# Performance work log

Measured on AMD Instinct MI355X. Metric: run time of the kernel, lower is better.

The kernel has to match this reference:

```python
import jax, jax.numpy as jnp
import numpy as np

N_HEAD = 16
T0 = 1.0        # eta schedule reference time
C_LOG = 3.0     # fixed eta(t) = C_LOG * log(t / T0)  (mode='log', non-learnable default)
ETA_CLIP = 50.0 # eta clamped to [-ETA_CLIP, ETA_CLIP] before exponentiation


def setup_inputs() -> dict:
    key = jax.random.key(0)
    k0, k1, k2 = jax.random.split(key, 3)
    B, T, D = 2, 2048, 1024
    x = jax.random.normal(k0, (B, T, D), dtype=jnp.float32)
    ln_weight = jnp.ones((D,), dtype=jnp.float32)  # LayerNorm weight (bias=False per cfg)
    c_attn_w = jax.random.normal(k1, (3 * D, D), dtype=jnp.float32) * 0.02  # torch Linear weight [3D, D]
    c_proj_w = jax.random.normal(k2, (D, D), dtype=jnp.float32) * 0.02      # output proj [D, D]
    # theta_h = inv_softplus(1.0) so that step size h = softplus(theta_h) = 1.0
    theta_h = jnp.asarray(np.log(np.expm1(1.0)), dtype=jnp.float32)
    return {"x": x, "ln_weight": ln_weight, "c_attn_w": c_attn_w,
            "c_proj_w": c_proj_w, "theta_h": theta_h}


def _layer_norm(x, w, eps=1e-5):
    mu = jnp.mean(x, axis=-1, keepdims=True)
    var = jnp.var(x, axis=-1, keepdims=True)
    return (x - mu) * jax.lax.rsqrt(var + eps) * w


def reference(x, ln_weight, c_attn_w, c_proj_w, theta_h):
    B, T, D = x.shape
    H = N_HEAD
    hd = D // H

    y = _layer_norm(x, ln_weight)
    qkv = jnp.einsum('btd,ed->bte', y, c_attn_w)        # [B, T, 3D]
    q, k, v = jnp.split(qkv, 3, axis=-1)
    q = q.reshape(B, T, H, hd).transpose(0, 2, 1, 3)    # [B, H, T, hd]
    k = k.reshape(B, T, H, hd).transpose(0, 2, 1, 3)
    v = v.reshape(B, T, H, hd).transpose(0, 2, 1, 3)

    # time-dependent conformal/symplectic scaling: t_i = t0 + h*i, eta = c_log*log(t/t0)
    h = jax.nn.softplus(theta_h)
    t = T0 + h * jnp.arange(T, dtype=jnp.float32)
    eta = jnp.clip(C_LOG * jnp.log(t / T0), -ETA_CLIP, ETA_CLIP)  # [T]
    q = q * jnp.exp(eta)[None, None, :, None]    # query scaled by exp(+eta(t_i))
    k = k * jnp.exp(-eta)[None, None, :, None]   # key scaled by exp(-eta(t_j))

    att = jnp.einsum('bhqd,bhkd->bhqk', q, k) / jnp.sqrt(jnp.float32(hd))
    mask = jnp.tril(jnp.ones((T, T), dtype=bool))  # causal: keep j <= i
    att = jnp.where(mask[None, None], att, -jnp.inf)
    att = jax.nn.softmax(att, axis=-1)

    out = jnp.einsum('bhqk,bhkd->bhqd', att, v)
    out = out.transpose(0, 2, 1, 3).reshape(B, T, D)
    return jnp.einsum('btd,ed->bte', out, c_proj_w)
```

## Files before the change

kernel.cpp:

```cpp
#include <hip/hip_runtime.h>
#include <stdint.h>
#include <stddef.h>

typedef __attribute__((ext_vector_type(8))) short short8;
typedef __attribute__((ext_vector_type(4))) float float4v;

#define T_SEQ 2048
#define D_MODEL 1024
#define NH 16
#define HD 64

static __device__ __forceinline__ unsigned short f2bf(float f) {
  unsigned u = __builtin_bit_cast(unsigned, f);
  u += 0x7fffu + ((u >> 16) & 1u);
  return (unsigned short)(u >> 16);
}
static __device__ __forceinline__ float bf2f(unsigned short h) {
  unsigned u = ((unsigned)h) << 16;
  return __builtin_bit_cast(float, u);
}
static __device__ __forceinline__ float4v mfma16(short8 a, short8 b, float4v c) {
  return __builtin_amdgcn_mfma_f32_16x16x32_bf16(a, b, c, 0, 0, 0);
}
static __device__ __forceinline__ void split3(float f, unsigned short& h0,
                                              unsigned short& h1, unsigned short& h2) {
  h0 = f2bf(f);
  float r1 = f - bf2f(h0);
  h1 = f2bf(r1);
  float r2 = r1 - bf2f(h1);
  h2 = f2bf(r2);
}
static __device__ __forceinline__ void split2(float f, unsigned short& h0, unsigned short& h1) {
  h0 = f2bf(f);
  h1 = f2bf(f - bf2f(h0));
}

static __device__ __forceinline__ void stage16(const unsigned short* g, unsigned short* l) {
#if __has_builtin(__builtin_amdgcn_global_load_lds)
  __builtin_amdgcn_global_load_lds(
      (const __attribute__((address_space(1))) unsigned int*)g,
      (__attribute__((address_space(3))) unsigned int*)l, 16, 0, 0);
#else
  *(short8*)l = *(const short8*)g;
#endif
}

__global__ __launch_bounds__(256) void prep_kernel(
    const float* x, const float* wgt, const float* attn_w, const float* theta,
    unsigned short* y0, unsigned short* y1, unsigned short* y2,
    unsigned short* W0, unsigned short* W1, unsigned short* W2,
    float* E, float* Einv) {
  __shared__ float rs[4], rq[4];
  int bx = blockIdx.x;
  int tid = threadIdx.x;
  if (bx < 4096) {
    int row = bx;
    const float* xr = x + (size_t)row * D_MODEL;
    float v[4];
    float sum = 0.f, ssq = 0.f;
    for (int it = 0; it < 4; ++it) {
      float f = xr[tid + 256 * it];
      v[it] = f;
      sum += f; ssq += f * f;
    }
    for (int off = 32; off >= 1; off >>= 1) {
      sum += __shfl_xor(sum, off, 64);
      ssq += __shfl_xor(ssq, off, 64);
    }
    int w = tid >> 6;
    if ((tid & 63) == 0) { rs[w] = sum; rq[w] = ssq; }
    __syncthreads();
    sum = rs[0] + rs[1] + rs[2] + rs[3];
    ssq = rq[0] + rq[1] + rq[2] + rq[3];
    float mu = sum * (1.0f / D_MODEL);
    float var = ssq * (1.0f / D_MODEL) - mu * mu;
    float rstd = rsqrtf(var + 1e-5f);
    for (int it = 0; it < 4; ++it) {
      int d = tid + 256 * it;
      float y = (v[it] - mu) * rstd * wgt[d];
      unsigned short h0, h1, h2;
      split3(y, h0, h1, h2);
      size_t o = (size_t)row * D_MODEL + d;
      y0[o] = h0; y1[o] = h1; y2[o] = h2;
    }
  } else if (bx < 5632) {
    size_t base = ((size_t)(bx - 4096) * 256 + tid) * 8;
    int row = (int)(base >> 10);
    short8 a, b, c;
    for (int j = 0; j < 8; ++j) {
      unsigned short h0, h1, h2;
      split3(attn_w[base + j], h0, h1, h2);
      a[j] = (short)h0; b[j] = (short)h1; c[j] = (short)h2;
    }
    *(short8*)(W0 + base) = a;
    *(short8*)(W1 + base) = b;
    if (row < 2048) *(short8*)(W2 + base) = c;
  } else {
    int i = (bx - 5632) * 256 + tid;
    if (i < T_SEQ) {
      float th = theta[0];
      float h = log1pf(expf(th));
      float t = 1.0f + h * (float)i;
      float eta = 3.0f * logf(t);
      eta = fminf(fmaxf(eta, -50.0f), 50.0f);
      E[i] = expf(eta);
      Einv[i] = expf(-eta);
    }
  }
}

__global__ __launch_bounds__(256) void conv_pw(const float* src, unsigned short* P0,
                                               unsigned short* P1) {
  size_t base = ((size_t)blockIdx.x * 256 + threadIdx.x) * 8;
  short8 a, b;
  for (int j = 0; j < 8; ++j) {
    unsigned short h0, h1;
    split2(src[base + j], h0, h1);
    a[j] = (short)h0; b[j] = (short)h1;
  }
  *(short8*)(P0 + base) = a;
  *(short8*)(P1 + base) = b;
}


#define RD_A(BUF, MF)                                                           \
  (*(const short8*)(lds_u + (BUF) * 12288 + (wm * 64 + (MF) * 16 + ln) * 32 +   \
                    slot8))
#define RD_B(BUF, NF)                                                           \
  (*(const short8*)(lds_u + (BUF) * 12288 + 8192 +                              \
                    (wn * 64 + (NF) * 16 + ln) * 32 + slot8))

#define STG(BUF, AP, BP, KI)                                                    \
  do {                                                                          \
    const unsigned short* ga = (AP) + (size_t)(m0 + srow) * 1024 + (KI) + kswz8; \
    stage16(ga, lds_u + (BUF) * 12288 + tid * 8);                               \
    stage16(ga + 128 * 1024, lds_u + (BUF) * 12288 + 4096 + tid * 8);           \
    stage16((BP) + (size_t)(brow0 + srow) * 1024 + (KI) + kswz8,                \
            lds_u + (BUF) * 12288 + 8192 + tid * 8);                            \
  } while (0)

#define ASEL(tb) ((tb) == 5 ? y2 : (((tb) & 1) ? y1 : y0))
#define BSEL(tb) (isV ? ((tb) < 2 ? W0 : W1)                                    \
                      : ((tb) < 2 ? W0 : ((tb) < 4 ? W1 : ((tb) == 4 ? W2 : W0))))

#define SBAR __builtin_amdgcn_s_barrier()
#define SCHED0 __builtin_amdgcn_sched_barrier(0)

#define PHASE(BUF, PBUF)                                                        \
  {                                                                             \
    short8 a0 = RD_A(BUF, 0), a1 = RD_A(BUF, 1);                                \
    short8 a2 = RD_A(BUF, 2), a3 = RD_A(BUF, 3);                                \
    short8 b0 = RD_B(BUF, 0), b1 = RD_B(BUF, 1);                                \
    short8 b2 = RD_B(BUF, 2), b3 = RD_B(BUF, 3);                                \
    bool pref = (t + 2 < NKT);                                                  \
    if (pref) {                                                                 \
      int tt = t + 2, tb = tt >> 5, ki = (tt & 31) << 5;                        \
      const unsigned short* Ap = ASEL(tb);                                      \
      const unsigned short* Bp = BSEL(tb);                                      \
      STG(PBUF, Ap, Bp, ki);                                                    \
    }                                                                           \
    SCHED0; SBAR;                                                               \
    asm volatile("s_waitcnt lgkmcnt(0)" ::: "memory");                          \
    SCHED0;                                                                     \
    __builtin_amdgcn_s_setprio(1);                                              \
    acc[0][0] = mfma16(a0, b0, acc[0][0]);                                      \
    acc[0][1] = mfma16(a0, b1, acc[0][1]);                                      \
    acc[0][2] = mfma16(a0, b2, acc[0][2]);                                      \
    acc[0][3] = mfma16(a0, b3, acc[0][3]);                                      \
    acc[1][0] = mfma16(a1, b0, acc[1][0]);                                      \
    acc[1][1] = mfma16(a1, b1, acc[1][1]);                                      \
    acc[1][2] = mfma16(a1, b2, acc[1][2]);                                      \
    acc[1][3] = mfma16(a1, b3, acc[1][3]);                                      \
    acc[2][0] = mfma16(a2, b0, acc[2][0]);                                      \
    acc[2][1] = mfma16(a2, b1, acc[2][1]);                                      \
    acc[2][2] = mfma16(a2, b2, acc[2][2]);                                      \
    acc[2][3] = mfma16(a2, b3, acc[2][3]);                                      \
    acc[3][0] = mfma16(a3, b0, acc[3][0]);                                      \
    acc[3][1] = mfma16(a3, b1, acc[3][1]);                                      \
    acc[3][2] = mfma16(a3, b2, acc[3][2]);                                      \
    acc[3][3] = mfma16(a3, b3, acc[3][3]);                                      \
    __builtin_amdgcn_s_setprio(0);                                              \
    SCHED0;                                                                     \
    if (pref) { asm volatile("s_waitcnt vmcnt(3)" ::: "memory"); }              \
    else      { asm volatile("s_waitcnt vmcnt(0)" ::: "memory"); }              \
    SBAR;                                                                       \
    ++t;                                                                        \
  }

__global__ __launch_bounds__(512, 4) void qkv_ring(
    const unsigned short* __restrict__ y0, const unsigned short* __restrict__ y1,
    const unsigned short* __restrict__ y2, const unsigned short* __restrict__ W0,
    const unsigned short* __restrict__ W1, const unsigned short* __restrict__ W2,
    const float* __restrict__ E, const float* __restrict__ Einv,
    float* __restrict__ Qf, unsigned short* __restrict__ K0,
    unsigned short* __restrict__ K1, unsigned short* __restrict__ K2,
    unsigned short* __restrict__ VbT) {
  extern __shared__ unsigned short lds_u[];
  int tid = threadIdx.x;
  int w = tid >> 6, lane = tid & 63, q4 = lane >> 4, ln = lane & 15;
  int wm = w >> 1, wn = w & 1;
  int slot8 = (q4 ^ ((ln >> 1) & 3)) * 8;
  int srow = tid >> 2;
  int kswz8 = ((tid & 3) ^ ((srow >> 1) & 3)) * 8;

  int bid = blockIdx.x, bx, by;
  if (bid < 256) {
    int wg = ((bid & 7) << 5) | (bid >> 3);
    by = wg >> 4; bx = wg & 15;
  } else {
    int vid = bid - 256;
    int wg = ((vid & 7) << 4) | (vid >> 3);
    by = wg >> 3; bx = 16 + (wg & 7);
  }
  int m0 = by * 256;
  bool isV = (bx >= 16);
  int NKT = isV ? 96 : 192;
  int brow0 = isV ? (2048 + (bx - 16) * 128) : bx * 128;

  float4v zero = {0.f, 0.f, 0.f, 0.f};
  float4v acc[4][4];
#pragma unroll
  for (int mf = 0; mf < 4; ++mf)
#pragma unroll
    for (int nf = 0; nf < 4; ++nf) acc[mf][nf] = zero;

  {
    const unsigned short* Ap = ASEL(0);
    const unsigned short* Bp = BSEL(0);
    STG(0, Ap, Bp, 0);
    STG(1, Ap, Bp, 32);
  }
  asm volatile("s_waitcnt vmcnt(3)" ::: "memory");
  SBAR;

  int t = 0;
  int nit = NKT / 3;
  for (int it = 0; it < nit; ++it) {
    PHASE(0, 2)
    PHASE(1, 0)
    PHASE(2, 1)
  }

  int bi = m0 >> 11, m0g = m0 & 2047;
  if (bx < 8) {
    float* Ql = (float*)lds_u;
    for (int g = 0; g < 2; ++g) {
      if (wn == g) {
#pragma unroll
        for (int mf = 0; mf < 4; ++mf)
#pragma unroll
          for (int nf = 0; nf < 4; ++nf)
#pragma unroll
            for (int r = 0; r < 4; ++r) {
              int rl = wm * 64 + mf * 16 + q4 * 4 + r;
              int tg = m0g + rl;
              Ql[rl * 64 + nf * 16 + ln] = acc[mf][nf][r] * (E[tg] * 0.1803368801f);
            }
      }
      __syncthreads();
      int h = bx * 2 + g;
      float* dst = Qf + ((size_t)(bi * NH + h) * T_SEQ + m0g) * HD;
      for (int itc = 0; itc < 8; ++itc) {
        int idx = itc * 512 + tid;
        *(float4v*)(dst + idx * 4) = *(const float4v*)(Ql + idx * 4);
      }
      __syncthreads();
    }
  } else if (bx < 16) {
    unsigned short* Kl = lds_u;
    for (int g = 0; g < 2; ++g)
      for (int half = 0; half < 2; ++half) {
        if (wn == g && (wm >> 1) == half) {
#pragma unroll
          for (int mf = 0; mf < 4; ++mf)
#pragma unroll
            for (int nf = 0; nf < 4; ++nf)
#pragma unroll
              for (int r = 0; r < 4; ++r) {
                int rlh = (wm & 1) * 64 + mf * 16 + q4 * 4 + r;
                int tg = m0g + half * 128 + rlh;
                unsigned short h0, h1, h2;
                split3(acc[mf][nf][r] * Einv[tg], h0, h1, h2);
                int o = rlh * 64 + nf * 16 + ln;
                Kl[o] = h0; Kl[8192 + o] = h1; Kl[16384 + o] = h2;
              }
        }
        __syncthreads();
        int h = (bx - 8) * 2 + g;
        size_t base = ((size_t)(bi * NH + h) * T_SEQ + m0g + half * 128) * HD;
        for (int itc = 0; itc < 2; ++itc) {
          int idx = itc * 512 + tid;
          *(short8*)(K0 + base + idx * 8) = *(const short8*)(Kl + idx * 8);
          *(short8*)(K1 + base + idx * 8) = *(const short8*)(Kl + 8192 + idx * 8);
          *(short8*)(K2 + base + idx * 8) = *(const short8*)(Kl + 16384 + idx * 8);
        }
        __syncthreads();
      }
  } else {
    unsigned short* Vl = lds_u;
    for (int g = 0; g < 2; ++g) {
      if (wn == g) {
#pragma unroll
        for (int mf = 0; mf < 4; ++mf)
#pragma unroll
          for (int nf = 0; nf < 4; ++nf)
#pragma unroll
            for (int r = 0; r < 4; ++r) {
              int rl = wm * 64 + mf * 16 + q4 * 4 + r;
              int d = nf * 16 + ln;
              Vl[d * 256 + rl] = f2bf(acc[mf][nf][r]);
            }
      }
      __syncthreads();
      int h = (bx - 16) * 2 + g;
      unsigned short* dst = VbT + (size_t)(bi * NH + h) * HD * T_SEQ + m0g;
      for (int itc = 0; itc < 4; ++itc) {
        int idx = itc * 512 + tid;
        int d = idx >> 5, c = idx & 31;
        *(short8*)(dst + (size_t)d * T_SEQ + c * 8) = *(const short8*)(Vl + d * 256 + c * 8);
      }
      __syncthreads();
    }
  }
}
#undef RD_A
#undef RD_B
#undef STG
#undef ASEL
#undef BSEL
#undef PHASE
#undef SBAR
#undef SCHED0

#define ATTN_STAGE(BUF, J0)                                                   \
  for (int i_ = 0; i_ < 2; ++i_) {                                            \
    size_t go_ = (size_t)((J0) + srow + i_ * 32) * 64 + scd * 8;              \
    int lo_ = tid * 8 + i_ * 2048;                                            \
    stage16(Kb0 + go_, &Ks[BUF][0][lo_]);                                     \
    stage16(Kb1 + go_, &Ks[BUF][1][lo_]);                                     \
    stage16(Kb2 + go_, &Ks[BUF][2][lo_]);                                     \
    stage16(Vb + (size_t)(srow + i_ * 32) * T_SEQ + (J0) + scd * 8,           \
            &Vs[BUF][lo_]);                                                   \
  }

#define ATTN_STEP(JT, DIAG)                                                   \
  {                                                                           \
    const int cur_ = (JT) & 1;                                                \
    float p[4][4];                                                            \
    for (int c = 0; c < 4; ++c) {                                             \
      float4v s = zero;                                                       \
      for (int ks = 0; ks < 2; ++ks) {                                        \
        int koff = ((c * 16 + ln) * 8 + ((ks * 4 + q4) ^ swz)) * 8;           \
        short8 k0v = *(const short8*)&Ks[cur_][0][koff];                      \
        short8 k1v = *(const short8*)&Ks[cur_][1][koff];                      \
        short8 k2v = *(const short8*)&Ks[cur_][2][koff];                      \
        s = mfma16(qa[ks][0], k0v, s);                                        \
        s = mfma16(qa[ks][1], k0v, s);                                        \
        s = mfma16(qa[ks][0], k1v, s);                                        \
        s = mfma16(qa[ks][1], k1v, s);                                        \
        s = mfma16(qa[ks][0], k2v, s);                                        \
        s = mfma16(qa[ks][2], k0v, s);                                        \
      }                                                                       \
      if (DIAG) {                                                             \
        int jrow = (JT) * 64 + c * 16 + ln;                                   \
        for (int r = 0; r < 4; ++r)                                           \
          if (jrow > ibase + q4 * 4 + r) s[r] = -3e38f;                       \
      }                                                                       \
      for (int r = 0; r < 4; ++r) p[c][r] = s[r];                             \
    }                                                                         \
    float tmx[4];                                                             \
    for (int r = 0; r < 4; ++r) {                                             \
      float tm = fmaxf(fmaxf(p[0][r], p[1][r]), fmaxf(p[2][r], p[3][r]));     \
      for (int off = 8; off >= 1; off >>= 1)                                  \
        tm = fmaxf(tm, __shfl_xor(tm, off, 16));                              \
      tmx[r] = tm;                                                            \
    }                                                                         \
    float grow = fmaxf(fmaxf(tmx[0] - m_r[0], tmx[1] - m_r[1]),               \
                       fmaxf(tmx[2] - m_r[2], tmx[3] - m_r[3]));              \
    if (!__all(grow <= 0.0f)) {                                               \
      float alpha[4];                                                         \
      for (int r = 0; r < 4; ++r) {                                           \
        float mnew = fmaxf(m_r[r], tmx[r]);                                   \
        alpha[r] = exp2f(m_r[r] - mnew);                                      \
        m_r[r] = mnew;                                                        \
      }                                                                       \
      for (int c = 0; c < 4; ++c)                                             \
        for (int r = 0; r < 4; ++r) oacc[c][r] *= alpha[r];                   \
      for (int r = 0; r < 4; ++r) lacc[r] *= alpha[r];                        \
    }                                                                         \
    for (int c = 0; c < 4; ++c)                                               \
      for (int r = 0; r < 4; ++r) p[c][r] = exp2f(p[c][r] - m_r[r]);          \
    __asm__ __volatile__("" ::: "memory");                                    \
    for (int c = 0; c < 4; ++c)                                               \
      for (int r = 0; r < 4; ++r)                                             \
        Plds[w][q4 * 4 + r][c * 16 + ln] =                                    \
            (unsigned short)(__builtin_bit_cast(unsigned, p[c][r]) >> 16);    \
    __asm__ __volatile__("" ::: "memory");                                    \
    for (int ks = 0; ks < 2; ++ks) {                                          \
      short8 pa = *(const short8*)&Plds[w][ln][ks * 32 + q4 * 8];             \
      for (int c = 0; c < 4; ++c) {                                           \
        int voff = ((c * 16 + ln) * 8 + ((ks * 4 + q4) ^ swz)) * 8;           \
        short8 vb = *(const short8*)&Vs[cur_][voff];                          \
        oacc[c] = mfma16(pa, vb, oacc[c]);                                    \
      }                                                                       \
      lacc = mfma16(pa, ones, lacc);                                          \
    }                                                                         \
    __asm__ __volatile__("" ::: "memory");                                    \
  }

__global__ __launch_bounds__(256) void attn_kernel(
    const float* Qf, const unsigned short* K0, const unsigned short* K1,
    const unsigned short* K2, const unsigned short* VbT,
    unsigned short* Ob0, unsigned short* Ob1) {
  __shared__ unsigned short Ks[2][3][4096];
  __shared__ unsigned short Vs[2][4096];
  __shared__ unsigned short Plds[4][16][72];
  int tid = threadIdx.x;
  int w = tid >> 6, lane = tid & 63, q4 = lane >> 4, ln = lane & 15;
  int bidx = blockIdx.x;
  int bh = ((bidx & 7) << 2) | ((bidx >> 3) & 3);
  int px = bidx >> 5;
  const float* Qb = Qf + (size_t)bh * T_SEQ * HD;
  const unsigned short* Kb0 = K0 + (size_t)bh * T_SEQ * HD;
  const unsigned short* Kb1 = K1 + (size_t)bh * T_SEQ * HD;
  const unsigned short* Kb2 = K2 + (size_t)bh * T_SEQ * HD;
  const unsigned short* Vb = VbT + (size_t)bh * HD * T_SEQ;
  int b = bh >> 4, hh = bh & 15;
  float4v zero = {0.f, 0.f, 0.f, 0.f};
  short8 ones;
  for (int j = 0; j < 8; ++j) ones[j] = (short)(unsigned short)0x3F80;

  int srow = tid >> 3, scs = tid & 7;
  int scd = scs ^ (srow & 7);
  int swz = ln & 7;

  for (int half = 0; half < 2; ++half) {
    int qt = half ? (31 - px) : px;
    int q0 = qt * 64;
    int ibase = q0 + w * 16;

    short8 qa[2][3];
    {
      const float* qp = Qb + (size_t)(ibase + ln) * HD;
      for (int ks = 0; ks < 2; ++ks) {
        float f[8];
        *(float4v*)&f[0] = *(const float4v*)(qp + ks * 32 + q4 * 8);
        *(float4v*)&f[4] = *(const float4v*)(qp + ks * 32 + q4 * 8 + 4);
        for (int j = 0; j < 8; ++j) {
          unsigned short h0, h1, h2;
          split3(f[j], h0, h1, h2);
          qa[ks][0][j] = (short)h0; qa[ks][1][j] = (short)h1; qa[ks][2][j] = (short)h2;
        }
      }
    }

    float m_r[4] = {-3e38f, -3e38f, -3e38f, -3e38f};
    float4v lacc = zero;
    float4v oacc[4];
    for (int c = 0; c < 4; ++c) oacc[c] = zero;

    __syncthreads();
    ATTN_STAGE(0, 0)
    for (int jt = 0; jt < qt; ++jt) {
      __syncthreads();
      ATTN_STAGE((jt + 1) & 1, (jt + 1) * 64)
      ATTN_STEP(jt, 0)
    }
    __syncthreads();
    ATTN_STEP(qt, 1)

    for (int c = 0; c < 4; ++c)
      for (int r = 0; r < 4; ++r) {
        int i = ibase + q4 * 4 + r;
        float val = oacc[c][r] / lacc[r];
        unsigned short h0, h1;
        split2(val, h0, h1);
        size_t o = ((size_t)(b * T_SEQ + i)) * D_MODEL + hh * 64 + c * 16 + ln;
        Ob0[o] = h0; Ob1[o] = h1;
      }
  }
}
#undef ATTN_STAGE
#undef ATTN_STEP

__global__ __launch_bounds__(256) void proj_gemm(
    const unsigned short* A0, const unsigned short* A1,
    const unsigned short* P0, const unsigned short* P1, float* out) {
  __shared__ unsigned short SB[4 * 4096];
  int tid = threadIdx.x;
  int w = tid >> 6, lane = tid & 63, q4 = lane >> 4, ln = lane & 15;
  int wr = w >> 1, wc = w & 1;
  int n0g = blockIdx.x * 128;
  int m0 = blockIdx.y * 128;
  const unsigned short* Asrc[2] = {A0, A1};
  const unsigned short* Bsrc[2] = {P0, P1};

  float4v zero = {0.f, 0.f, 0.f, 0.f};
  float4v acc[4][4];
  for (int mt = 0; mt < 4; ++mt)
    for (int ct = 0; ct < 4; ++ct) acc[mt][ct] = zero;

  int srow = tid >> 2, kpart = tid & 3;
  int kswz = kpart ^ ((srow >> 1) & 3);
  int slot8 = (q4 ^ ((ln >> 1) & 3)) * 8;
  unsigned lds_off = (unsigned)tid * 16;

  for (int k0 = 0; k0 < D_MODEL; k0 += 32) {
    __syncthreads();
    for (int i = 0; i < 2; ++i) {
      size_t arow = (size_t)(m0 + srow + i * 64) * D_MODEL + k0 + kswz * 8;
      size_t brow = (size_t)(n0g + srow + i * 64) * D_MODEL + k0 + kswz * 8;
      for (int s = 0; s < 2; ++s) {
        stage16(Asrc[s] + arow, (unsigned short*)((char*)(SB + s * 4096) + lds_off + i * 4096));
        stage16(Bsrc[s] + brow, (unsigned short*)((char*)(SB + (2 + s) * 4096) + lds_off + i * 4096));
      }
    }
    __syncthreads();

    short8 af[4][2];
    for (int mt = 0; mt < 4; ++mt)
      for (int s = 0; s < 2; ++s)
        af[mt][s] = *(const short8*)(SB + s * 4096 + (wr * 64 + mt * 16 + ln) * 32 + slot8);
    for (int ct = 0; ct < 4; ++ct) {
      int brow = (wc * 64 + ct * 16 + ln) * 32 + slot8;
      short8 b0 = *(const short8*)(SB + 2 * 4096 + brow);
      short8 b1 = *(const short8*)(SB + 3 * 4096 + brow);
      for (int mt = 0; mt < 4; ++mt) {
        float4v a = acc[mt][ct];
        a = mfma16(af[mt][0], b0, a);
        a = mfma16(af[mt][1], b0, a);
        a = mfma16(af[mt][0], b1, a);
        acc[mt][ct] = a;
      }
    }
  }

  for (int mt = 0; mt < 4; ++mt)
    for (int ct = 0; ct < 4; ++ct)
      for (int r = 0; r < 4; ++r) {
        int gm = m0 + wr * 64 + mt * 16 + q4 * 4 + r;
        int col = n0g + wc * 64 + ct * 16 + ln;
        out[(size_t)gm * D_MODEL + col] = acc[mt][ct][r];
      }
}

extern "C" void kernel_launch(void* const* d_in, const int* in_sizes, int n_in,
                              void* d_out, int out_size, void* d_ws, size_t ws_size,
                              hipStream_t stream) {
  const float* x      = (const float*)d_in[0];
  const float* ln_w   = (const float*)d_in[1];
  const float* attn_w = (const float*)d_in[2];
  const float* proj_w = (const float*)d_in[3];
  const float* theta  = (const float*)d_in[4];
  float* out = (float*)d_out;

  char* ws = (char*)d_ws;
  const size_t SZY  = (size_t)4096 * 1024 * 2;
  const size_t SZW  = (size_t)3072 * 1024 * 2;
  const size_t SZW2 = (size_t)2048 * 1024 * 2;
  const size_t SZQ  = (size_t)2 * 16 * 2048 * 64 * 4;
  const size_t SZK  = (size_t)2 * 16 * 2048 * 64 * 2;

  unsigned short* y0 = (unsigned short*)(ws);
  unsigned short* y1 = (unsigned short*)(ws + SZY);
  unsigned short* y2 = (unsigned short*)(ws + 2 * SZY);
  unsigned short* W0 = (unsigned short*)(ws + 3 * SZY);
  unsigned short* W1 = (unsigned short*)(ws + 3 * SZY + SZW);
  unsigned short* W2 = (unsigned short*)(ws + 3 * SZY + 2 * SZW);
  float* Qf          = (float*)(ws + 3 * SZY + 2 * SZW + SZW2);
  unsigned short* K0 = (unsigned short*)(ws + 3 * SZY + 2 * SZW + SZW2 + SZQ);
  unsigned short* K1 = (unsigned short*)(ws + 3 * SZY + 2 * SZW + SZW2 + SZQ + SZK);
  float* E           = (float*)(ws + 3 * SZY + 2 * SZW + SZW2 + SZQ + 2 * SZK);
  float* Einv        = E + T_SEQ;
  unsigned short* Ob0 = y0;
  unsigned short* Ob1 = y1;
  unsigned short* PW0 = y2;
  unsigned short* PW1 = y2 + (size_t)1024 * 1024;
  unsigned short* VbT = (unsigned short*)d_out;
  unsigned short* K2  = (unsigned short*)((char*)d_out + SZK);

  size_t needed = 3 * SZY + 2 * SZW + SZW2 + SZQ + 2 * SZK + 2 * T_SEQ * 4;
  if (ws_size < needed) return;

  static int lds_cfg = 0;
  if (!lds_cfg) {
    hipFuncSetAttribute((const void*)qkv_ring,
                        hipFuncAttributeMaxDynamicSharedMemorySize, 73728);
    lds_cfg = 1;
  }

  prep_kernel<<<dim3(5640), dim3(256), 0, stream>>>(x, ln_w, attn_w, theta,
                                                    y0, y1, y2, W0, W1, W2, E, Einv);
  qkv_ring<<<dim3(384), dim3(512), 73728, stream>>>(y0, y1, y2, W0, W1, W2, E, Einv,
                                                    Qf, K0, K1, K2, VbT);
  conv_pw<<<dim3(512), dim3(256), 0, stream>>>(proj_w, PW0, PW1);
  attn_kernel<<<dim3(512), dim3(256), 0, stream>>>(Qf, K0, K1, K2, VbT, Ob0, Ob1);
  proj_gemm<<<dim3(8, 32), dim3(256), 0, stream>>>(Ob0, Ob1, PW0, PW1, out);
}
```

Before: 381.2 us.

## Split V projection into narrower 256x64 tiles with dedicated pipeline

V-projection blocks now compute 256x64 tiles (one head each) instead of 256x128, doubling V blocks so the grid grows from 384 to 512 workgroups. A separate PHASE_V pipeline gives each wave a 32x64 sub-tile with half the MFMAs per step, and only half the threads stage B, with adjusted vmcnt waits. The aim is better load balance across CUs, since V blocks previously did half the K-steps of Q/K blocks. The cost is lower arithmetic intensity for V tiles and more redundant A-tile loads.

```diff
diff --git a/kernel.cpp b/kernel.cpp
--- a/kernel.cpp
+++ b/kernel.cpp
@@ -140,8 +140,7 @@
   } while (0)
 
 #define ASEL(tb) ((tb) == 5 ? y2 : (((tb) & 1) ? y1 : y0))
-#define BSEL(tb) (isV ? ((tb) < 2 ? W0 : W1)                                    \
-                      : ((tb) < 2 ? W0 : ((tb) < 4 ? W1 : ((tb) == 4 ? W2 : W0))))
+#define BSELQK(tb) ((tb) < 2 ? W0 : ((tb) < 4 ? W1 : ((tb) == 4 ? W2 : W0)))
 
 #define SBAR __builtin_amdgcn_s_barrier()
 #define SCHED0 __builtin_amdgcn_sched_barrier(0)
@@ -152,11 +151,11 @@
     short8 a2 = RD_A(BUF, 2), a3 = RD_A(BUF, 3);                                \
     short8 b0 = RD_B(BUF, 0), b1 = RD_B(BUF, 1);                                \
     short8 b2 = RD_B(BUF, 2), b3 = RD_B(BUF, 3);                                \
-    bool pref = (t + 2 < NKT);                                                  \
+    bool pref = (t + 2 < 192);                                                  \
     if (pref) {                                                                 \
       int tt = t + 2, tb = tt >> 5, ki = (tt & 31) << 5;                        \
       const unsigned short* Ap = ASEL(tb);                                      \
-      const unsigned short* Bp = BSEL(tb);                                      \
+      const unsigned short* Bp = BSELQK(tb);                                    \
       STG(PBUF, Ap, Bp, ki);                                                    \
     }                                                                           \
     SCHED0; SBAR;                                                               \
@@ -187,6 +186,57 @@
     ++t;                                                                        \
   }
 
+#define RD_AV(BUF, MF)                                                          \
+  (*(const short8*)(lds_u + (BUF) * 12288 + (w * 32 + (MF) * 16 + ln) * 32 +    \
+                    slot8))
+#define RD_BV(BUF, NF)                                                          \
+  (*(const short8*)(lds_u + (BUF) * 12288 + 8192 + ((NF) * 16 + ln) * 32 +      \
+                    slot8))
+
+#define STG_V(BUF, AP, BP, KI)                                                  \
+  do {                                                                          \
+    const unsigned short* ga = (AP) + (size_t)(m0 + srow) * 1024 + (KI) + kswz8; \
+    stage16(ga, lds_u + (BUF) * 12288 + tid * 8);                               \
+    stage16(ga + 128 * 1024, lds_u + (BUF) * 12288 + 4096 + tid * 8);           \
+    if (tid < 256)                                                              \
+      stage16((BP) + (size_t)(brow0 + srow) * 1024 + (KI) + kswz8,              \
+              lds_u + (BUF) * 12288 + 8192 + tid * 8);                          \
+  } while (0)
+
+#define PHASE_V(BUF, PBUF)                                                      \
+  {                                                                             \
+    short8 a0 = RD_AV(BUF, 0), a1 = RD_AV(BUF, 1);                              \
+    short8 b0 = RD_BV(BUF, 0), b1 = RD_BV(BUF, 1);                              \
+    short8 b2 = RD_BV(BUF, 2), b3 = RD_BV(BUF, 3);                              \
+    bool pref = (t + 2 < 96);                                                   \
+    if (pref) {                                                                 \
+      int tt = t + 2, tb = tt >> 5, ki = (tt & 31) << 5;                        \
+      const unsigned short* Ap = (tb & 1) ? y1 : y0;                            \
+      const unsigned short* Bp = (tb < 2) ? W0 : W1;                            \
+      STG_V(PBUF, Ap, Bp, ki);                                                  \
+    }                                                                           \
+    SCHED0; SBAR;                                                               \
+    asm volatile("s_waitcnt lgkmcnt(0)" ::: "memory");                          \
+    SCHED0;                                                                     \
+    __builtin_amdgcn_s_setprio(1);                                              \
+    acc2[0][0] = mfma16(a0, b0, acc2[0][0]);                                    \
+    acc2[0][1] = mfma16(a0, b1, acc2[0][1]);                                    \
+    acc2[0][2] = mfma16(a0, b2, acc2[0][2]);                                    \
+    acc2[0][3] = mfma16(a0, b3, acc2[0][3]);                                    \
+    acc2[1][0] = mfma16(a1, b0, acc2[1][0]);                                    \
+    acc2[1][1] = mfma16(a1, b1, acc2[1][1]);                                    \
+    acc2[1][2] = mfma16(a1, b2, acc2[1][2]);                                    \
+    acc2[1][3] = mfma16(a1, b3, acc2[1][3]);                                    \
+    __builtin_amdgcn_s_setprio(0);                                              \
+    SCHED0;                                                                     \
+    if (pref) {                                                                 \
+      if (w < 4) { asm volatile("s_waitcnt vmcnt(3)" ::: "memory"); }           \
+      else       { asm volatile("s_waitcnt vmcnt(2)" ::: "memory"); }           \
+    } else { asm volatile("s_waitcnt vmcnt(0)" ::: "memory"); }                 \
+    SBAR;                                                                       \
+    ++t;                                                                        \
+  }
+
 __global__ __launch_bounds__(512, 4) void qkv_ring(
     const unsigned short* __restrict__ y0, const unsigned short* __restrict__ y1,
     const unsigned short* __restrict__ y2, const unsigned short* __restrict__ W0,
@@ -209,117 +259,131 @@
     by = wg >> 4; bx = wg & 15;
   } else {
     int vid = bid - 256;
-    int wg = ((vid & 7) << 4) | (vid >> 3);
-    by = wg >> 3; bx = 16 + (wg & 7);
+    int wg = ((vid & 7) << 5) | (vid >> 3);
+    by = wg >> 4; bx = 16 + (wg & 15);
   }
   int m0 = by * 256;
   bool isV = (bx >= 16);
-  int NKT = isV ? 96 : 192;
-  int brow0 = isV ? (2048 + (bx - 16) * 128) : bx * 128;
-
+  int brow0 = isV ? (2048 + (bx - 16) * 64) : bx * 128;
+  int bi = m0 >> 11, m0g = m0 & 2047;
   float4v zero = {0.f, 0.f, 0.f, 0.f};
-  float4v acc[4][4];
-#pragma unroll
-  for (int mf = 0; mf < 4; ++mf)
-#pragma unroll
-    for (int nf = 0; nf < 4; ++nf) acc[mf][nf] = zero;
-
-  {
-    const unsigned short* Ap = ASEL(0);
-    const unsigned short* Bp = BSEL(0);
-    STG(0, Ap, Bp, 0);
-    STG(1, Ap, Bp, 32);
-  }
-  asm volatile("s_waitcnt vmcnt(3)" ::: "memory");
-  SBAR;
-
-  int t = 0;
-  int nit = NKT / 3;
-  for (int it = 0; it < nit; ++it) {
-    PHASE(0, 2)
-    PHASE(1, 0)
-    PHASE(2, 1)
-  }
-
-  int bi = m0 >> 11, m0g = m0 & 2047;
-  if (bx < 8) {
-    float* Ql = (float*)lds_u;
-    for (int g = 0; g < 2; ++g) {
-      if (wn == g) {
-#pragma unroll
-        for (int mf = 0; mf < 4; ++mf)
-#pragma unroll
-          for (int nf = 0; nf < 4; ++nf)
-#pragma unroll
-            for (int r = 0; r < 4; ++r) {
-              int rl = wm * 64 + mf * 16 + q4 * 4 + r;
-              int tg = m0g + rl;
-              Ql[rl * 64 + nf * 16 + ln] = acc[mf][nf][r] * (E[tg] * 0.1803368801f);
-            }
-      }
-      __syncthreads();
-      int h = bx * 2 + g;
-      float* dst = Qf + ((size_t)(bi * NH + h) * T_SEQ + m0g) * HD;
-      for (int itc = 0; itc < 8; ++itc) {
-        int idx = itc * 512 + tid;
-        *(float4v*)(dst + idx * 4) = *(const float4v*)(Ql + idx * 4);
-      }
-      __syncthreads();
-    }
-  } else if (bx < 16) {
-    unsigned short* Kl = lds_u;
-    for (int g = 0; g < 2; ++g)
-      for (int half = 0; half < 2; ++half) {
-        if (wn == g && (wm >> 1) == half) {
+
+  if (!isV) {
+    float4v acc[4][4];
+#pragma unroll
+    for (int mf = 0; mf < 4; ++mf)
+#pragma unroll
+      for (int nf = 0; nf < 4; ++nf) acc[mf][nf] = zero;
+
+    {
+      const unsigned short* Ap = ASEL(0);
+      const unsigned short* Bp = BSELQK(0);
+      STG(0, Ap, Bp, 0);
+      STG(1, Ap, Bp, 32);
+    }
+    asm volatile("s_waitcnt vmcnt(3)" ::: "memory");
+    SBAR;
+
+    int t = 0;
+    for (int it = 0; it < 64; ++it) {
+      PHASE(0, 2)
+      PHASE(1, 0)
+      PHASE(2, 1)
+    }
+
+    if (bx < 8) {
+      float* Ql = (float*)lds_u;
+      for (int g = 0; g < 2; ++g) {
+        if (wn == g) {
 #pragma unroll
           for (int mf = 0; mf < 4; ++mf)
 #pragma unroll
             for (int nf = 0; nf < 4; ++nf)
 #pragma unroll
               for (int r = 0; r < 4; ++r) {
-                int rlh = (wm & 1) * 64 + mf * 16 + q4 * 4 + r;
-                int tg = m0g + half * 128 + rlh;
-                unsigned short h0, h1, h2;
-                split3(acc[mf][nf][r] * Einv[tg], h0, h1, h2);
-                int o = rlh * 64 + nf * 16 + ln;
-                Kl[o] = h0; Kl[8192 + o] = h1; Kl[16384 + o] = h2;
+                int rl = wm * 64 + mf * 16 + q4 * 4 + r;
+                int tg = m0g + rl;
+                Ql[rl * 64 + nf * 16 + ln] = acc[mf][nf][r] * (E[tg] * 0.1803368801f);
               }
         }
         __syncthreads();
-        int h = (bx - 8) * 2 + g;
-        size_t base = ((size_t)(bi * NH + h) * T_SEQ + m0g + half * 128) * HD;
-        for (int itc = 0; itc < 2; ++itc) {
+        int h = bx * 2 + g;
+        float* dst = Qf + ((size_t)(bi * NH + h) * T_SEQ + m0g) * HD;
+        for (int itc = 0; itc < 8; ++itc) {
           int idx = itc * 512 + tid;
-          *(short8*)(K0 + base + idx * 8) = *(const short8*)(Kl + idx * 8);
-          *(short8*)(K1 + base + idx * 8) = *(const short8*)(Kl + 8192 + idx * 8);
-          *(short8*)(K2 + base + idx * 8) = *(const short8*)(Kl + 16384 + idx * 8);
+          *(float4v*)(dst + idx * 4) = *(const float4v*)(Ql + idx * 4);
         }
         __syncthreads();
       }
+    } else {
+      unsigned short* Kl = lds_u;
+      for (int g = 0; g < 2; ++g)
+        for (int half = 0; half < 2; ++half) {
+          if (wn == g && (wm >> 1) == half) {
+#pragma unroll
+            for (int mf = 0; mf < 4; ++mf)
+#pragma unroll
+              for (int nf = 0; nf < 4; ++nf)
+#pragma unroll
+                for (int r = 0; r < 4; ++r) {
+                  int rlh = (wm & 1) * 64 + mf * 16 + q4 * 4 + r;
+                  int tg = m0g + half * 128 + rlh;
+                  unsigned short h0, h1, h2;
+                  split3(acc[mf][nf][r] * Einv[tg], h0, h1, h2);
+                  int o = rlh * 64 + nf * 16 + ln;
+                  Kl[o] = h0; Kl[8192 + o] = h1; Kl[16384 + o] = h2;
+                }
+          }
+          __syncthreads();
+          int h = (bx - 8) * 2 + g;
+          size_t base = ((size_t)(bi * NH + h) * T_SEQ + m0g + half * 128) * HD;
+          for (int itc = 0; itc < 2; ++itc) {
+            int idx = itc * 512 + tid;
+            *(short8*)(K0 + base + idx * 8) = *(const short8*)(Kl + idx * 8);
+            *(short8*)(K1 + base + idx * 8) = *(const short8*)(Kl + 8192 + idx * 8);
+            *(short8*)(K2 + base + idx * 8) = *(const short8*)(Kl + 16384 + idx * 8);
+          }
+          __syncthreads();
+        }
+    }
   } else {
+    float4v acc2[2][4];
+#pragma unroll
+    for (int mf = 0; mf < 2; ++mf)
+#pragma unroll
+      for (int nf = 0; nf < 4; ++nf) acc2[mf][nf] = zero;
+
+    STG_V(0, y0, W0, 0);
+    STG_V(1, y0, W0, 32);
+    if (w < 4) { asm volatile("s_waitcnt vmcnt(3)" ::: "memory"); }
+    else       { asm volatile("s_waitcnt vmcnt(2)" ::: "memory"); }
+    SBAR;
+
+    int t = 0;
+    for (int it = 0; it < 32; ++it) {
+      PHASE_V(0, 2)
+      PHASE_V(1, 0)
+      PHASE_V(2, 1)
+    }
+
     unsigned short* Vl = lds_u;
-    for (int g = 0; g < 2; ++g) {
-      if (wn == g) {
-#pragma unroll
-        for (int mf = 0; mf < 4; ++mf)
-#pragma unroll
-          for (int nf = 0; nf < 4; ++nf)
-#pragma unroll
-            for (int r = 0; r < 4; ++r) {
-              int rl = wm * 64 + mf * 16 + q4 * 4 + r;
-              int d = nf * 16 + ln;
-              Vl[d * 256 + rl] = f2bf(acc[mf][nf][r]);
-            }
-      }
-      __syncthreads();
-      int h = (bx - 16) * 2 + g;
-      unsigned short* dst = VbT + (size_t)(bi * NH + h) * HD * T_SEQ + m0g;
-      for (int itc = 0; itc < 4; ++itc) {
-        int idx = itc * 512 + tid;
-        int d = idx >> 5, c = idx & 31;
-        *(short8*)(dst + (size_t)d * T_SEQ + c * 8) = *(const short8*)(Vl + d * 256 + c * 8);
-      }
-      __syncthreads();
+#pragma unroll
+    for (int mf = 0; mf < 2; ++mf)
+#pragma unroll
+      for (int nf = 0; nf < 4; ++nf)
+#pragma unroll
+        for (int r = 0; r < 4; ++r) {
+          int t_loc = w * 32 + mf * 16 + q4 * 4 + r;
+          int d = nf * 16 + ln;
+          Vl[d * 256 + t_loc] = f2bf(acc2[mf][nf][r]);
+        }
+    __syncthreads();
+    int h = bx - 16;
+    unsigned short* dst = VbT + (size_t)(bi * NH + h) * HD * T_SEQ + m0g;
+    for (int itc = 0; itc < 4; ++itc) {
+      int idx = itc * 512 + tid;
+      int d = idx >> 5, c = idx & 31;
+      *(short8*)(dst + (size_t)d * T_SEQ + c * 8) = *(const short8*)(Vl + d * 256 + c * 8);
     }
   }
 }
@@ -327,8 +391,12 @@
 #undef RD_B
 #undef STG
 #undef ASEL
-#undef BSEL
+#undef BSELQK
 #undef PHASE
+#undef RD_AV
+#undef RD_BV
+#undef STG_V
+#undef PHASE_V
 #undef SBAR
 #undef SCHED0
 
@@ -591,7 +659,7 @@
 
   prep_kernel<<<dim3(5640), dim3(256), 0, stream>>>(x, ln_w, attn_w, theta,
                                                     y0, y1, y2, W0, W1, W2, E, Einv);
-  qkv_ring<<<dim3(384), dim3(512), 73728, stream>>>(y0, y1, y2, W0, W1, W2, E, Einv,
+  qkv_ring<<<dim3(512), dim3(512), 73728, stream>>>(y0, y1, y2, W0, W1, W2, E, Einv,
                                                     Qf, K0, K1, K2, VbT);
   conv_pw<<<dim3(512), dim3(256), 0, stream>>>(proj_w, PW0, PW1);
   attn_kernel<<<dim3(512), dim3(256), 0, stream>>>(Qf, K0, K1, K2, VbT, Ob0, Ob1);
```

New measurement: 370.4 us. 1.03x faster.
